# Kernel tuning notes

Measured on AMD Instinct MI355X. Metric: run time of the kernel, lower is better.

## Reference

```python
import jax, jax.numpy as jnp
import numpy as np
import math

H = 8  # n_heads

def rel_shift(x):
    # x: [B, H, U, P] -> Transformer-XL relative shift
    B, h, U, P = x.shape
    x = jnp.pad(x, ((0, 0), (0, 0), (0, 0), (1, 0)))  # zero-pad front of last dim
    x = x.reshape(B, h, P + 1, U)[:, :, 1:, :].reshape(B, h, U, P)
    return x

def setup_inputs() -> dict:
    key = jax.random.key(0)
    ks = jax.random.split(key, 16)
    B, T, D = 8, 1024, 512
    s = 0.05  # weight scale ~ xavier for D=512
    inp = {
        'q': jax.random.normal(ks[0], (B, T, D), jnp.float32),
        'k': jax.random.normal(ks[1], (B, T, D), jnp.float32),
        'v': jax.random.normal(ks[2], (B, T, D), jnp.float32),
        'pos': jax.random.normal(ks[3], (T, D), jnp.float32),
        'mask': jax.random.randint(ks[4], (B, T, T), 0, 2).astype(jnp.int32),
        'Wq': jax.random.normal(ks[5], (D, D), jnp.float32) * s,
        'bq': jnp.zeros((D,), jnp.float32),
        'Wk': jax.random.normal(ks[6], (D, D), jnp.float32) * s,
        'bk': jnp.zeros((D,), jnp.float32),
        'Wv': jax.random.normal(ks[7], (D, D), jnp.float32) * s,
        'bv': jnp.zeros((D,), jnp.float32),
        'Wo': jax.random.normal(ks[8], (D, D), jnp.float32) * s,
        'bo': jnp.zeros((D,), jnp.float32),
        'Wp': jax.random.normal(ks[9], (D, D), jnp.float32) * s,
        'bias_u': jax.random.normal(ks[10], (H, D // H), jnp.float32) * s,
        'bias_v': jax.random.normal(ks[11], (H, D // H), jnp.float32) * s,
    }
    return inp

def reference(q, k, v, pos, mask, Wq, bq, Wk, bk, Wv, bv, Wo, bo, Wp, bias_u, bias_v):
    B, T, D = q.shape
    dk = D // H
    qh = (q @ Wq.T + bq).reshape(B, T, H, dk)   # B U H d
    kh = (k @ Wk.T + bk).reshape(B, T, H, dk)   # B T H d
    vh = (v @ Wv.T + bv).reshape(B, T, H, dk)   # B T H d
    ph = (pos @ Wp.T).reshape(T, H, dk)          # P H d (shared across batch)
    q_u = qh + bias_u                            # B U H d
    q_v = qh + bias_v
    ac = jnp.einsum('buhd,bthd->bhut', q_u, kh)  # content term
    bd = jnp.einsum('buhd,phd->bhup', q_v, ph)   # position term
    bd = rel_shift(bd)[:, :, :, :T]
    scores = (ac + bd) / math.sqrt(dk)           # B H U T
    m = (mask[:, None, :, :] == 0)               # B 1 U T
    neg = jnp.finfo(scores.dtype).min
    scores = jnp.where(m, neg, scores)
    attn = jax.nn.softmax(scores, axis=-1)
    attn = jnp.where(m, 0.0, attn)
    x = jnp.einsum('bhut,bthd->buhd', attn, vh).reshape(B, T, D)
    return x @ Wo.T + bo
```

## Files before the change

kernel.cpp:

```cpp
#include <hip/hip_runtime.h>
#include <stdint.h>

#define Bc 8
#define Tc 1024
#define Dc 512
#define Hc 8

typedef __bf16 bf16x8 __attribute__((ext_vector_type(8)));
typedef float f32x4 __attribute__((ext_vector_type(4)));
typedef unsigned short ushort8v __attribute__((ext_vector_type(8)));

#define NEGBF 0xF14Au

__device__ __forceinline__ unsigned short f2bf(float f) {
    union { float f; uint32_t u; } v; v.f = f;
    uint32_t u = v.u;
    u += 0x7fffu + ((u >> 16) & 1u);
    return (unsigned short)(u >> 16);
}
__device__ __forceinline__ unsigned short f2bf_native(float f) {
    __bf16 b = (__bf16)f;
    return *(unsigned short*)&b;
}
__device__ __forceinline__ f32x4 mfma16(bf16x8 a, bf16x8 b, f32x4 c) {
    return __builtin_amdgcn_mfma_f32_16x16x32_bf16(a, b, c, 0, 0, 0);
}
__device__ __forceinline__ void gl16(const unsigned short* g, unsigned short* l) {
    __builtin_amdgcn_global_load_lds(
        (const __attribute__((address_space(1))) uint32_t*)g,
        (__attribute__((address_space(3))) uint32_t*)l, 16, 0, 0);
}

#define SC2 0.1803368801f
#define THR2 11.541560327f

__global__ __launch_bounds__(256) void prep(
    const int* __restrict__ mask, uint32_t* __restrict__ bits,
    const float* __restrict__ Wq, const float* __restrict__ Wk,
    const float* __restrict__ Wv, const float* __restrict__ Wp,
    const float* __restrict__ Wo, unsigned short* __restrict__ Wb,
    const float* __restrict__ q, const float* __restrict__ k,
    const float* __restrict__ v, const float* __restrict__ p,
    unsigned short* __restrict__ qb, unsigned short* __restrict__ kb,
    unsigned short* __restrict__ vb, unsigned short* __restrict__ pb)
{
    int bid = blockIdx.x;
    if (bid < 32768) {
        int wid = (bid * 256 + threadIdx.x) >> 6;
        int lane = threadIdx.x & 63;
        unsigned long long bl = __ballot(mask[(size_t)wid * 64 + lane] != 0);
        if (lane == 0)  bits[wid * 2]     = (uint32_t)bl;
        if (lane == 32) bits[wid * 2 + 1] = (uint32_t)(bl >> 32);
    } else if (bid < 33408) {
        int i = (bid - 32768) * 2048 + threadIdx.x * 8;
        int m = i >> 18, r = i & 262143;
        const float* Ws[5] = {Wq, Wk, Wv, Wp, Wo};
        const float* s = Ws[m] + r;
        ushort8v o;
#pragma unroll
        for (int j = 0; j < 8; ++j) o[j] = f2bf(s[j]);
        *(ushort8v*)(Wb + i) = o;
    } else {
        size_t i = (size_t)(bid - 33408) * 2048 + threadIdx.x * 8;
        const float* src; unsigned short* dst; size_t off;
        if (i < 4194304)       { src = q; dst = qb; off = i; }
        else if (i < 8388608)  { src = k; dst = kb; off = i - 4194304; }
        else if (i < 12582912) { src = v; dst = vb; off = i - 8388608; }
        else                   { src = p; dst = pb; off = i - 12582912; }
        ushort8v o;
#pragma unroll
        for (int j = 0; j < 8; ++j) o[j] = f2bf(src[off + j]);
        *(ushort8v*)(dst + off) = o;
    }
}

__global__ __launch_bounds__(256) void proj4(
    const unsigned short* __restrict__ qb, const unsigned short* __restrict__ kb,
    const unsigned short* __restrict__ vb, const unsigned short* __restrict__ pb,
    const unsigned short* __restrict__ Wb,
    const float* __restrict__ bq, const float* __restrict__ bk,
    const float* __restrict__ bv,
    const float* __restrict__ bias_u, const float* __restrict__ bias_v,
    unsigned short* __restrict__ qu, unsigned short* __restrict__ qv,
    unsigned short* __restrict__ kh, unsigned short* __restrict__ vT,
    unsigned short* __restrict__ ph)
{
    int id = blockIdx.x;
    int wg = (id & 7) * 100 + (id >> 3);
    int z, rem;
    if (wg < 256)      { z = 0; rem = wg; }
    else if (wg < 512) { z = 1; rem = wg - 256; }
    else if (wg < 768) { z = 2; rem = wg - 512; }
    else               { z = 3; rem = wg - 768; }
    const int m0 = (rem & 3) * 128, n0 = (rem >> 2) * 128;
    const unsigned short* A = z == 0 ? qb : z == 1 ? kb : z == 2 ? vb : pb;
    const unsigned short* W = Wb + (size_t)z * 262144;

    __shared__ unsigned short As[128][64];
    __shared__ unsigned short Bs[128][64];
    const int tid = threadIdx.x, lane = tid & 63, wave = tid >> 6;
    const int lrow = lane & 15, lkg = lane >> 4;
    const int wr = (wave >> 1) * 64, wc = (wave & 1) * 64;
    const int srow = lane >> 3, scol = (lane & 7) * 8;

    f32x4 acc[4][4];
#pragma unroll
    for (int i = 0; i < 4; ++i)
#pragma unroll
        for (int j = 0; j < 4; ++j) acc[i][j] = f32x4{0.f, 0.f, 0.f, 0.f};

    for (int kt = 0; kt < 512; kt += 64) {
        __syncthreads();
#pragma unroll
        for (int it = 0; it < 4; ++it) {
            int r8 = (wave * 4 + it) * 8;
            gl16(A + (size_t)(n0 + r8 + srow) * 512 + kt + scol, &As[r8][0]);
            gl16(W + (size_t)(m0 + r8 + srow) * 512 + kt + scol, &Bs[r8][0]);
        }
        __syncthreads();
#pragma unroll
        for (int kk = 0; kk < 2; ++kk) {
            bf16x8 a[4], bb[4];
#pragma unroll
            for (int i = 0; i < 4; ++i)
                a[i] = *(const bf16x8*)&As[wr + i * 16 + lrow][kk * 32 + lkg * 8];
#pragma unroll
            for (int j = 0; j < 4; ++j)
                bb[j] = *(const bf16x8*)&Bs[wc + j * 16 + lrow][kk * 32 + lkg * 8];
#pragma unroll
            for (int i = 0; i < 4; ++i)
#pragma unroll
                for (int j = 0; j < 4; ++j)
                    acc[i][j] = mfma16(a[i], bb[j], acc[i][j]);
        }
    }

#pragma unroll
    for (int i = 0; i < 4; ++i) {
        int nbase = n0 + wr + i * 16 + lkg * 4;
#pragma unroll
        for (int j = 0; j < 4; ++j) {
            int m = m0 + wc + j * 16 + lrow;
            float bb = z == 0 ? bq[m] : z == 1 ? bk[m] : z == 2 ? bv[m] : 0.f;
            float bu = 0.f, bvv = 0.f;
            if (z == 0) { bu = bias_u[m]; bvv = bias_v[m]; }
#pragma unroll
            for (int qq = 0; qq < 4; ++qq) {
                int n = nbase + qq;
                float c = acc[i][j][qq] + bb;
                if (z == 0) {
                    qu[(size_t)n * 512 + m] = f2bf(c + bu);
                    qv[(size_t)n * 512 + m] = f2bf(c + bvv);
                } else if (z == 1) {
                    kh[(size_t)n * 512 + m] = f2bf(c * SC2);
                } else if (z == 2) {
                    int b = n >> 10, t = n & 1023, h = m >> 6, d = m & 63;
                    vT[(((size_t)((b * 8 + h) * 64 + d)) << 10) + t] = f2bf(c);
                } else {
                    ph[(size_t)n * 512 + m] = f2bf(c);
                }
            }
        }
    }
}

__global__ __launch_bounds__(256) void gemm_out(
    const unsigned short* __restrict__ X, const unsigned short* __restrict__ Wob,
    const float* __restrict__ bo, float* __restrict__ fout)
{
    int id = blockIdx.x;
    int wg = (id & 7) * 32 + (id >> 3);
    const int m0 = (wg & 3) * 128, n0 = (wg >> 2) * 128;
    __shared__ unsigned short As[128][64];
    __shared__ unsigned short Bs[128][64];
    const int tid = threadIdx.x, lane = tid & 63, wave = tid >> 6;
    const int lrow = lane & 15, lkg = lane >> 4;
    const int wr = (wave >> 1) * 64, wc = (wave & 1) * 64;
    const int srow = lane >> 3, scol = (lane & 7) * 8;

    f32x4 acc[4][4];
#pragma unroll
    for (int i = 0; i < 4; ++i)
#pragma unroll
        for (int j = 0; j < 4; ++j) acc[i][j] = f32x4{0.f, 0.f, 0.f, 0.f};

    for (int kt = 0; kt < 512; kt += 64) {
        __syncthreads();
#pragma unroll
        for (int it = 0; it < 4; ++it) {
            int r8 = (wave * 4 + it) * 8;
            gl16(X   + (size_t)(n0 + r8 + srow) * 512 + kt + scol, &As[r8][0]);
            gl16(Wob + (size_t)(m0 + r8 + srow) * 512 + kt + scol, &Bs[r8][0]);
        }
        __syncthreads();
#pragma unroll
        for (int kk = 0; kk < 2; ++kk) {
            bf16x8 a[4], bb[4];
#pragma unroll
            for (int i = 0; i < 4; ++i)
                a[i] = *(const bf16x8*)&As[wr + i * 16 + lrow][kk * 32 + lkg * 8];
#pragma unroll
            for (int j = 0; j < 4; ++j)
                bb[j] = *(const bf16x8*)&Bs[wc + j * 16 + lrow][kk * 32 + lkg * 8];
#pragma unroll
            for (int i = 0; i < 4; ++i)
#pragma unroll
                for (int j = 0; j < 4; ++j)
                    acc[i][j] = mfma16(a[i], bb[j], acc[i][j]);
        }
    }
#pragma unroll
    for (int i = 0; i < 4; ++i) {
        int nbase = n0 + wr + i * 16 + lkg * 4;
#pragma unroll
        for (int j = 0; j < 4; ++j) {
            int m = m0 + wc + j * 16 + lrow;
            float bb = bo[m];
#pragma unroll
            for (int qq = 0; qq < 4; ++qq)
                fout[(size_t)(nbase + qq) * 512 + m] = acc[i][j][qq] + bb;
        }
    }
}

__global__ __launch_bounds__(256) void bd_gemm(
    const unsigned short* __restrict__ qv, const unsigned short* __restrict__ ph,
    const uint32_t* __restrict__ mbits, unsigned short* __restrict__ bds,
    int bh_base)
{
    int id = blockIdx.x, wg;
    if (gridDim.x == 4096) wg = (id & 7) * 512 + (id >> 3);
    else                   wg = (id & 7) * 64 + (id >> 3);
    const int zz = wg >> 6, rem = wg & 63;
    const int u0 = (rem & 7) * 128, p0 = (rem >> 3) * 128;
    const int bh = bh_base + zz;
    const int b = bh >> 3, h = bh & 7;
    __shared__ unsigned short As[128][64];
    __shared__ unsigned short Bs[128][64];
    const int tid = threadIdx.x, lane = tid & 63, wave = tid >> 6;
    const int lrow = lane & 15, lkg = lane >> 4;
    const int wr = (wave >> 1) * 64, wc = (wave & 1) * 64;
    const int srow = lane >> 3, scol = (lane & 7) * 8;

#pragma unroll
    for (int it = 0; it < 4; ++it) {
        int r8 = (wave * 4 + it) * 8;
        gl16(qv + ((size_t)(b * 1024 + u0 + r8 + srow)) * 512 + h * 64 + scol, &As[r8][0]);
        gl16(ph + ((size_t)(p0 + r8 + srow)) * 512 + h * 64 + scol, &Bs[r8][0]);
    }
    __syncthreads();

    f32x4 acc[4][4];
#pragma unroll
    for (int i = 0; i < 4; ++i)
#pragma unroll
        for (int j = 0; j < 4; ++j) acc[i][j] = f32x4{0.f, 0.f, 0.f, 0.f};
#pragma unroll
    for (int kk = 0; kk < 2; ++kk) {
        bf16x8 a[4], bb[4];
#pragma unroll
        for (int i = 0; i < 4; ++i)
            a[i] = *(const bf16x8*)&As[wr + i * 16 + lrow][kk * 32 + lkg * 8];
#pragma unroll
        for (int j = 0; j < 4; ++j)
            bb[j] = *(const bf16x8*)&Bs[wc + j * 16 + lrow][kk * 32 + lkg * 8];
#pragma unroll
        for (int i = 0; i < 4; ++i)
#pragma unroll
            for (int j = 0; j < 4; ++j)
                acc[i][j] = mfma16(a[i], bb[j], acc[i][j]);
    }

    unsigned short* slab = bds + ((size_t)zz << 20);
    const uint32_t* mb = mbits + ((size_t)b << 15);
    const int Cbase = 1025 * (u0 + wr + lkg * 4) + (p0 + wc + lrow) - 1023;
#pragma unroll
    for (int i = 0; i < 4; ++i) {
#pragma unroll
        for (int qq = 0; qq < 4; ++qq) {
            int Fb = Cbase + 1025 * (i * 16 + qq);
            int w0 = Fb >> 5;
            uint32_t mw0 = mb[w0], mw1 = mb[w0 + 1], mw2 = mb[w0 + 2];
            uint64_t m01 = ((uint64_t)mw1 << 32) | mw0;
            uint64_t m12 = ((uint64_t)mw2 << 32) | mw1;
            int sh = Fb & 31;
#pragma unroll
            for (int j = 0; j < 4; ++j) {
                uint32_t bit = (j < 2) ? ((uint32_t)(m01 >> (sh + j * 16)) & 1u)
                                       : ((uint32_t)(m12 >> (sh + (j - 2) * 16)) & 1u);
                unsigned short val = bit ? f2bf_native(acc[i][j][qq] * SC2)
                                         : (unsigned short)NEGBF;
                int F = Fb + j * 16;
                if (F >= 0) slab[F] = val;
            }
        }
    }

    if (p0 == 0 && tid < 128) {
        int ud = u0 + tid;
        if (ud < 1023) {
            const uint8_t* mrowbytes = (const uint8_t*)mbits + ((size_t)b << 17);
            uint32_t bit = (mrowbytes[ud * 128 + ((ud + 1) >> 3)] >> ((ud + 1) & 7)) & 1;
            slab[((size_t)ud << 10) + (ud + 1)] = bit ? 0 : (unsigned short)NEGBF;
        }
    }
}

__global__ __launch_bounds__(256, 4) void attn6(
    const unsigned short* __restrict__ qu, const unsigned short* __restrict__ kh,
    const unsigned short* __restrict__ vT, const unsigned short* __restrict__ bds,
    unsigned short* __restrict__ xout, int b_base)
{
    int id = blockIdx.x, nid, b, rem;
    if (gridDim.x == 1024) {
        nid = (id & 7) * 128 + (id >> 3);
        b = b_base + (nid >> 7); rem = nid & 127;
    } else {
        nid = (id & 7) * 16 + (id >> 3);
        b = b_base; rem = nid;
    }
    const int h = rem >> 4, ublk = rem & 15;
    const int u0 = ublk * 64;

    __shared__ unsigned short Ks[64][64];
    __shared__ unsigned short Vs[64][64];
    __shared__ unsigned short Ps[4][16][72];
    const int tid = threadIdx.x, lane = tid & 63, wave = tid >> 6;
    const int lrow = lane & 15, lkg = lane >> 4;
    const int srow = lane >> 3;
    const int scol = ((lane & 7) ^ (srow & 7)) * 8;
    const int swr  = (lrow & 7) * 8;
    const f32x4 zero = {0.f, 0.f, 0.f, 0.f};

    const unsigned short* qub = qu + ((size_t)(b * 1024 + u0 + wave * 16 + lrow)) * 512 + h * 64;
    bf16x8 au0 = *(const bf16x8*)(qub + lkg * 8);
    bf16x8 au1 = *(const bf16x8*)(qub + 32 + lkg * 8);

    const int urow = u0 + wave * 16 + lkg * 4;
    const int zoff = (b - b_base) * 8 + h;
    const unsigned short* bdp[4];
#pragma unroll
    for (int q = 0; q < 4; ++q)
        bdp[q] = bds + ((size_t)zoff << 20) + (((size_t)(urow + q)) << 10) + lrow;
    const unsigned short* kbase = kh + ((size_t)(b * 1024)) * 512 + h * 64;
    const unsigned short* vbase = vT + (((size_t)((b * 8 + h) * 64)) << 10);

    f32x4 acc[4] = {zero, zero, zero, zero};
    float mrow[4], lsum[4];
#pragma unroll
    for (int q = 0; q < 4; ++q) { mrow[q] = -3.0e38f; lsum[q] = 0.f; }

    for (int t0 = 0; t0 < 1024; t0 += 64) {
        __syncthreads();
#pragma unroll
        for (int it = 0; it < 2; ++it) {
            int r8 = (wave * 2 + it) * 8;
            gl16(kbase + (size_t)(t0 + r8 + srow) * 512 + scol, &Ks[r8][0]);
            gl16(vbase + ((size_t)(r8 + srow) << 10) + t0 + scol, &Vs[r8][0]);
        }
        f32x4 bdC[4];
#pragma unroll
        for (int j = 0; j < 4; ++j)
#pragma unroll
            for (int q = 0; q < 4; ++q)
                bdC[j][q] = __uint_as_float(((uint32_t)bdp[q][j * 16]) << 16);
#pragma unroll
        for (int q = 0; q < 4; ++q) bdp[q] += 64;
        __syncthreads();

        f32x4 s[4];
#pragma unroll
        for (int j = 0; j < 4; ++j) {
            bf16x8 k0 = *(const bf16x8*)&Ks[j * 16 + lrow][(lkg * 8) ^ swr];
            bf16x8 k1 = *(const bf16x8*)&Ks[j * 16 + lrow][(32 + lkg * 8) ^ swr];
            s[j] = mfma16(au1, k1, mfma16(au0, k0, bdC[j]));
        }
        float lmax[4];
#pragma unroll
        for (int q = 0; q < 4; ++q)
            lmax[q] = fmaxf(fmaxf(s[0][q], s[1][q]), fmaxf(s[2][q], s[3][q]));
        int need = (lmax[0] > mrow[0] + THR2) | (lmax[1] > mrow[1] + THR2) |
                   (lmax[2] > mrow[2] + THR2) | (lmax[3] > mrow[3] + THR2);
        if (__any(need)) {
            float rmx[4] = {lmax[0], lmax[1], lmax[2], lmax[3]};
#pragma unroll
            for (int off = 1; off < 16; off <<= 1)
#pragma unroll
                for (int q = 0; q < 4; ++q) rmx[q] = fmaxf(rmx[q], __shfl_xor(rmx[q], off));
#pragma unroll
            for (int q = 0; q < 4; ++q) {
                float mn = fmaxf(mrow[q], rmx[q]);
                float fr = exp2f(mrow[q] - mn);
                mrow[q] = mn;
                lsum[q] *= fr;
#pragma unroll
                for (int jj = 0; jj < 4; ++jj) acc[jj][q] *= fr;
            }
        }
#pragma unroll
        for (int j = 0; j < 4; ++j) {
#pragma unroll
            for (int q = 0; q < 4; ++q) {
                float p = exp2f(s[j][q] - mrow[q]);
                lsum[q] += p;
                Ps[wave][lkg * 4 + q][j * 16 + lrow] = f2bf_native(p);
            }
        }
        bf16x8 pa0 = *(const bf16x8*)&Ps[wave][lrow][lkg * 8];
        bf16x8 pa1 = *(const bf16x8*)&Ps[wave][lrow][32 + lkg * 8];
#pragma unroll
        for (int jj = 0; jj < 4; ++jj) {
            bf16x8 vb0 = *(const bf16x8*)&Vs[jj * 16 + lrow][(lkg * 8) ^ swr];
            bf16x8 vb1 = *(const bf16x8*)&Vs[jj * 16 + lrow][(32 + lkg * 8) ^ swr];
            acc[jj] = mfma16(pa1, vb1, mfma16(pa0, vb0, acc[jj]));
        }
    }

#pragma unroll
    for (int off = 1; off < 16; off <<= 1)
#pragma unroll
        for (int q = 0; q < 4; ++q) lsum[q] += __shfl_xor(lsum[q], off);
#pragma unroll
    for (int q = 0; q < 4; ++q) {
        float inv = 1.0f / lsum[q];
        int u = urow + q;
#pragma unroll
        for (int jj = 0; jj < 4; ++jj) {
            int d = jj * 16 + lrow;
            xout[((size_t)(b * 1024 + u)) * 512 + h * 64 + d] = f2bf_native(acc[jj][q] * inv);
        }
    }
}

extern "C" void kernel_launch(void* const* d_in, const int* in_sizes, int n_in,
                              void* d_out, int out_size, void* d_ws, size_t ws_size,
                              hipStream_t stream) {
    const float* q    = (const float*)d_in[0];
    const float* k    = (const float*)d_in[1];
    const float* v    = (const float*)d_in[2];
    const float* pos  = (const float*)d_in[3];
    const int*   mask = (const int*)d_in[4];
    const float* Wq   = (const float*)d_in[5];
    const float* bq   = (const float*)d_in[6];
    const float* Wk   = (const float*)d_in[7];
    const float* bk   = (const float*)d_in[8];
    const float* Wv   = (const float*)d_in[9];
    const float* bv   = (const float*)d_in[10];
    const float* Wo   = (const float*)d_in[11];
    const float* bo   = (const float*)d_in[12];
    const float* Wp   = (const float*)d_in[13];
    const float* bias_u = (const float*)d_in[14];
    const float* bias_v = (const float*)d_in[15];
    float* out = (float*)d_out;

    unsigned short* ws = (unsigned short*)d_ws;
    constexpr size_t NQ  = (size_t)Bc * Tc * Dc;
    constexpr size_t NP  = (size_t)Tc * Dc;
    constexpr size_t NMB = (size_t)Bc * Tc * 32;
    constexpr size_t NWB = (size_t)5 * 262144;
    unsigned short* ws_qu = ws;
    unsigned short* ws_qv = ws_qu + NQ;
    unsigned short* ws_kh = ws_qv + NQ;
    unsigned short* ws_vT = ws_kh + NQ;
    unsigned short* ws_ph = ws_vT + NQ;
    uint32_t*       ws_mb = (uint32_t*)(ws_ph + NP);
    unsigned short* ws_wb = (unsigned short*)(ws_mb + NMB);
    unsigned short* ws_qb = ws_wb + NWB;
    unsigned short* ws_kb = ws_qb + NQ;
    unsigned short* ws_vb = ws_kb + NQ;
    unsigned short* ws_pb = ws_vb + NQ;
    unsigned short* ws_bd = ws_qb;

    constexpr size_t BD_FULL  = (size_t)64 * 1024 * 1024;
    constexpr size_t BD_SMALL = (size_t)8 * 1024 * 1024;
    const size_t base_bytes = (4 * NQ + NP + NWB) * 2 + NMB * 4;
    const bool full  = ws_size >= base_bytes + BD_FULL * 2;
    const bool tier2 = !full && ws_size >= base_bytes + ((3 * NQ + NP) + NQ) * 2;

    dim3 blk(256);
    prep<<<39808, blk, 0, stream>>>(mask, ws_mb, Wq, Wk, Wv, Wp, Wo, ws_wb,
                                    q, k, v, pos, ws_qb, ws_kb, ws_vb, ws_pb);
    proj4<<<800, blk, 0, stream>>>(ws_qb, ws_kb, ws_vb, ws_pb, ws_wb, bq, bk, bv,
                                   bias_u, bias_v, ws_qu, ws_qv, ws_kh, ws_vT, ws_ph);

    if (full) {
        unsigned short* ws_x = ws_qv;
        bd_gemm<<<4096, blk, 0, stream>>>(ws_qv, ws_ph, ws_mb, ws_bd, 0);
        attn6<<<1024, blk, 0, stream>>>(ws_qu, ws_kh, ws_vT, ws_bd, ws_x, 0);
        gemm_out<<<256, blk, 0, stream>>>(ws_x, ws_wb + 4 * 262144, bo, out);
    } else if (tier2) {
        unsigned short* ws_x = ws_qb + 3 * NQ + NP;
        for (int b = 0; b < 8; ++b) {
            bd_gemm<<<512, blk, 0, stream>>>(ws_qv, ws_ph, ws_mb, ws_bd, b * 8);
            attn6<<<128, blk, 0, stream>>>(ws_qu, ws_kh, ws_vT, ws_bd, ws_x, b);
        }
        gemm_out<<<256, blk, 0, stream>>>(ws_x, ws_wb + 4 * 262144, bo, out);
    }
}
```

Baseline: 189.3 us.

## Double-buffer LDS tiles in projection, output GEMM and attention kernels

Adds ping-pong shared-memory buffers to proj4, gemm_out and the attention kernel. The next K/V or A/W tile is prefetched while the current one is consumed, which leaves one barrier per iteration instead of two. The GEMMs also gain an XOR swizzle on LDS columns to avoid bank conflicts. In exchange, shared memory per block doubles, and the attention kernel's occupancy hint drops from 4 to 3 blocks per CU.

```diff
diff --git a/kernel.cpp b/kernel.cpp
--- a/kernel.cpp
+++ b/kernel.cpp
@@ -96,12 +96,14 @@
     const unsigned short* A = z == 0 ? qb : z == 1 ? kb : z == 2 ? vb : pb;
     const unsigned short* W = Wb + (size_t)z * 262144;
 
-    __shared__ unsigned short As[128][64];
-    __shared__ unsigned short Bs[128][64];
+    __shared__ unsigned short As[2][128][64];
+    __shared__ unsigned short Bs[2][128][64];
     const int tid = threadIdx.x, lane = tid & 63, wave = tid >> 6;
     const int lrow = lane & 15, lkg = lane >> 4;
     const int wr = (wave >> 1) * 64, wc = (wave & 1) * 64;
-    const int srow = lane >> 3, scol = (lane & 7) * 8;
+    const int srow = lane >> 3;
+    const int scol = ((lane & 7) ^ (srow & 7)) * 8;
+    const int swr  = (lrow & 7) * 8;
 
     f32x4 acc[4][4];
 #pragma unroll
@@ -109,30 +111,41 @@
 #pragma unroll
         for (int j = 0; j < 4; ++j) acc[i][j] = f32x4{0.f, 0.f, 0.f, 0.f};
 
+#pragma unroll
+    for (int it = 0; it < 4; ++it) {
+        int r8 = (wave * 4 + it) * 8;
+        gl16(A + (size_t)(n0 + r8 + srow) * 512 + scol, &As[0][r8][0]);
+        gl16(W + (size_t)(m0 + r8 + srow) * 512 + scol, &Bs[0][r8][0]);
+    }
+    __syncthreads();
+
+    int cur = 0;
     for (int kt = 0; kt < 512; kt += 64) {
-        __syncthreads();
-#pragma unroll
-        for (int it = 0; it < 4; ++it) {
-            int r8 = (wave * 4 + it) * 8;
-            gl16(A + (size_t)(n0 + r8 + srow) * 512 + kt + scol, &As[r8][0]);
-            gl16(W + (size_t)(m0 + r8 + srow) * 512 + kt + scol, &Bs[r8][0]);
-        }
-        __syncthreads();
+        if (kt + 64 < 512) {
+#pragma unroll
+            for (int it = 0; it < 4; ++it) {
+                int r8 = (wave * 4 + it) * 8;
+                gl16(A + (size_t)(n0 + r8 + srow) * 512 + kt + 64 + scol, &As[cur ^ 1][r8][0]);
+                gl16(W + (size_t)(m0 + r8 + srow) * 512 + kt + 64 + scol, &Bs[cur ^ 1][r8][0]);
+            }
+        }
 #pragma unroll
         for (int kk = 0; kk < 2; ++kk) {
             bf16x8 a[4], bb[4];
 #pragma unroll
             for (int i = 0; i < 4; ++i)
-                a[i] = *(const bf16x8*)&As[wr + i * 16 + lrow][kk * 32 + lkg * 8];
+                a[i] = *(const bf16x8*)&As[cur][wr + i * 16 + lrow][(kk * 32 + lkg * 8) ^ swr];
 #pragma unroll
             for (int j = 0; j < 4; ++j)
-                bb[j] = *(const bf16x8*)&Bs[wc + j * 16 + lrow][kk * 32 + lkg * 8];
+                bb[j] = *(const bf16x8*)&Bs[cur][wc + j * 16 + lrow][(kk * 32 + lkg * 8) ^ swr];
 #pragma unroll
             for (int i = 0; i < 4; ++i)
 #pragma unroll
                 for (int j = 0; j < 4; ++j)
                     acc[i][j] = mfma16(a[i], bb[j], acc[i][j]);
         }
+        __syncthreads();
+        cur ^= 1;
     }
 
 #pragma unroll
@@ -171,12 +184,14 @@
     int id = blockIdx.x;
     int wg = (id & 7) * 32 + (id >> 3);
     const int m0 = (wg & 3) * 128, n0 = (wg >> 2) * 128;
-    __shared__ unsigned short As[128][64];
-    __shared__ unsigned short Bs[128][64];
+    __shared__ unsigned short As[2][128][64];
+    __shared__ unsigned short Bs[2][128][64];
     const int tid = threadIdx.x, lane = tid & 63, wave = tid >> 6;
     const int lrow = lane & 15, lkg = lane >> 4;
     const int wr = (wave >> 1) * 64, wc = (wave & 1) * 64;
-    const int srow = lane >> 3, scol = (lane & 7) * 8;
+    const int srow = lane >> 3;
+    const int scol = ((lane & 7) ^ (srow & 7)) * 8;
+    const int swr  = (lrow & 7) * 8;
 
     f32x4 acc[4][4];
 #pragma unroll
@@ -184,30 +199,41 @@
 #pragma unroll
         for (int j = 0; j < 4; ++j) acc[i][j] = f32x4{0.f, 0.f, 0.f, 0.f};
 
+#pragma unroll
+    for (int it = 0; it < 4; ++it) {
+        int r8 = (wave * 4 + it) * 8;
+        gl16(X   + (size_t)(n0 + r8 + srow) * 512 + scol, &As[0][r8][0]);
+        gl16(Wob + (size_t)(m0 + r8 + srow) * 512 + scol, &Bs[0][r8][0]);
+    }
+    __syncthreads();
+
+    int cur = 0;
     for (int kt = 0; kt < 512; kt += 64) {
-        __syncthreads();
-#pragma unroll
-        for (int it = 0; it < 4; ++it) {
-            int r8 = (wave * 4 + it) * 8;
-            gl16(X   + (size_t)(n0 + r8 + srow) * 512 + kt + scol, &As[r8][0]);
-            gl16(Wob + (size_t)(m0 + r8 + srow) * 512 + kt + scol, &Bs[r8][0]);
-        }
-        __syncthreads();
+        if (kt + 64 < 512) {
+#pragma unroll
+            for (int it = 0; it < 4; ++it) {
+                int r8 = (wave * 4 + it) * 8;
+                gl16(X   + (size_t)(n0 + r8 + srow) * 512 + kt + 64 + scol, &As[cur ^ 1][r8][0]);
+                gl16(Wob + (size_t)(m0 + r8 + srow) * 512 + kt + 64 + scol, &Bs[cur ^ 1][r8][0]);
+            }
+        }
 #pragma unroll
         for (int kk = 0; kk < 2; ++kk) {
             bf16x8 a[4], bb[4];
 #pragma unroll
             for (int i = 0; i < 4; ++i)
-                a[i] = *(const bf16x8*)&As[wr + i * 16 + lrow][kk * 32 + lkg * 8];
+                a[i] = *(const bf16x8*)&As[cur][wr + i * 16 + lrow][(kk * 32 + lkg * 8) ^ swr];
 #pragma unroll
             for (int j = 0; j < 4; ++j)
-                bb[j] = *(const bf16x8*)&Bs[wc + j * 16 + lrow][kk * 32 + lkg * 8];
+                bb[j] = *(const bf16x8*)&Bs[cur][wc + j * 16 + lrow][(kk * 32 + lkg * 8) ^ swr];
 #pragma unroll
             for (int i = 0; i < 4; ++i)
 #pragma unroll
                 for (int j = 0; j < 4; ++j)
                     acc[i][j] = mfma16(a[i], bb[j], acc[i][j]);
         }
+        __syncthreads();
+        cur ^= 1;
     }
 #pragma unroll
     for (int i = 0; i < 4; ++i) {
@@ -306,7 +332,7 @@
     }
 }
 
-__global__ __launch_bounds__(256, 4) void attn6(
+__global__ __launch_bounds__(256, 3) void attn7(
     const unsigned short* __restrict__ qu, const unsigned short* __restrict__ kh,
     const unsigned short* __restrict__ vT, const unsigned short* __restrict__ bds,
     unsigned short* __restrict__ xout, int b_base)
@@ -322,8 +348,8 @@
     const int h = rem >> 4, ublk = rem & 15;
     const int u0 = ublk * 64;
 
-    __shared__ unsigned short Ks[64][64];
-    __shared__ unsigned short Vs[64][64];
+    __shared__ unsigned short Ks[2][64][64];
+    __shared__ unsigned short Vs[2][64][64];
     __shared__ unsigned short Ps[4][16][72];
     const int tid = threadIdx.x, lane = tid & 63, wave = tid >> 6;
     const int lrow = lane & 15, lkg = lane >> 4;
@@ -350,14 +376,16 @@
 #pragma unroll
     for (int q = 0; q < 4; ++q) { mrow[q] = -3.0e38f; lsum[q] = 0.f; }
 
+#pragma unroll
+    for (int it = 0; it < 2; ++it) {
+        int r8 = (wave * 2 + it) * 8;
+        gl16(kbase + (size_t)(r8 + srow) * 512 + scol, &Ks[0][r8][0]);
+        gl16(vbase + ((size_t)(r8 + srow) << 10) + scol, &Vs[0][r8][0]);
+    }
+    __syncthreads();
+
+    int cur = 0;
     for (int t0 = 0; t0 < 1024; t0 += 64) {
-        __syncthreads();
-#pragma unroll
-        for (int it = 0; it < 2; ++it) {
-            int r8 = (wave * 2 + it) * 8;
-            gl16(kbase + (size_t)(t0 + r8 + srow) * 512 + scol, &Ks[r8][0]);
-            gl16(vbase + ((size_t)(r8 + srow) << 10) + t0 + scol, &Vs[r8][0]);
-        }
         f32x4 bdC[4];
 #pragma unroll
         for (int j = 0; j < 4; ++j)
@@ -366,13 +394,21 @@
                 bdC[j][q] = __uint_as_float(((uint32_t)bdp[q][j * 16]) << 16);
 #pragma unroll
         for (int q = 0; q < 4; ++q) bdp[q] += 64;
-        __syncthreads();
+
+        if (t0 < 960) {
+#pragma unroll
+            for (int it = 0; it < 2; ++it) {
+                int r8 = (wave * 2 + it) * 8;
+                gl16(kbase + (size_t)(t0 + 64 + r8 + srow) * 512 + scol, &Ks[cur ^ 1][r8][0]);
+                gl16(vbase + ((size_t)(r8 + srow) << 10) + t0 + 64 + scol, &Vs[cur ^ 1][r8][0]);
+            }
+        }
 
         f32x4 s[4];
 #pragma unroll
         for (int j = 0; j < 4; ++j) {
-            bf16x8 k0 = *(const bf16x8*)&Ks[j * 16 + lrow][(lkg * 8) ^ swr];
-            bf16x8 k1 = *(const bf16x8*)&Ks[j * 16 + lrow][(32 + lkg * 8) ^ swr];
+            bf16x8 k0 = *(const bf16x8*)&Ks[cur][j * 16 + lrow][(lkg * 8) ^ swr];
+            bf16x8 k1 = *(const bf16x8*)&Ks[cur][j * 16 + lrow][(32 + lkg * 8) ^ swr];
             s[j] = mfma16(au1, k1, mfma16(au0, k0, bdC[j]));
         }
         float lmax[4];
@@ -410,10 +446,12 @@
         bf16x8 pa1 = *(const bf16x8*)&Ps[wave][lrow][32 + lkg * 8];
 #pragma unroll
         for (int jj = 0; jj < 4; ++jj) {
-            bf16x8 vb0 = *(const bf16x8*)&Vs[jj * 16 + lrow][(lkg * 8) ^ swr];
-            bf16x8 vb1 = *(const bf16x8*)&Vs[jj * 16 + lrow][(32 + lkg * 8) ^ swr];
+            bf16x8 vb0 = *(const bf16x8*)&Vs[cur][jj * 16 + lrow][(lkg * 8) ^ swr];
+            bf16x8 vb1 = *(const bf16x8*)&Vs[cur][jj * 16 + lrow][(32 + lkg * 8) ^ swr];
             acc[jj] = mfma16(pa1, vb1, mfma16(pa0, vb0, acc[jj]));
         }
+        __syncthreads();
+        cur ^= 1;
     }
 
 #pragma unroll
@@ -486,13 +524,13 @@
     if (full) {
         unsigned short* ws_x = ws_qv;
         bd_gemm<<<4096, blk, 0, stream>>>(ws_qv, ws_ph, ws_mb, ws_bd, 0);
-        attn6<<<1024, blk, 0, stream>>>(ws_qu, ws_kh, ws_vT, ws_bd, ws_x, 0);
+        attn7<<<1024, blk, 0, stream>>>(ws_qu, ws_kh, ws_vT, ws_bd, ws_x, 0);
         gemm_out<<<256, blk, 0, stream>>>(ws_x, ws_wb + 4 * 262144, bo, out);
     } else if (tier2) {
         unsigned short* ws_x = ws_qb + 3 * NQ + NP;
         for (int b = 0; b < 8; ++b) {
             bd_gemm<<<512, blk, 0, stream>>>(ws_qv, ws_ph, ws_mb, ws_bd, b * 8);
-            attn6<<<128, blk, 0, stream>>>(ws_qu, ws_kh, ws_vT, ws_bd, ws_x, b);
+            attn7<<<128, blk, 0, stream>>>(ws_qu, ws_kh, ws_vT, ws_bd, ws_x, b);
         }
         gemm_out<<<256, blk, 0, stream>>>(ws_x, ws_wb + 4 * 262144, bo, out);
     }
```

Result: no change. 190.9 us (+0.9%).
